# Kernel optimization log

Hardware: AMD Instinct MI355X
Metric: run time of the kernel (lower is better)

Reference implementation:

```python
import jax, jax.numpy as jnp
import numpy as np

B, S, E, H = 16, 512, 4096, 8
HD = E // H  # 512, must equal S for this module's math
LN_EPS = 1e-5
NORM_EPS = 1e-12


def setup_inputs() -> dict:
    key = jax.random.key(0)
    ks = jax.random.split(key, 16)
    s_e = 1.0 / np.sqrt(E)
    s_h = 1.0 / np.sqrt(HD)
    return {
        "x": jax.random.normal(ks[0], (B, S, E), jnp.float32),
        "Wq": jax.random.normal(ks[1], (E, E), jnp.float32) * s_e,
        "bq": jnp.zeros((E,), jnp.float32),
        "Wk": jax.random.normal(ks[2], (E, E), jnp.float32) * s_e,
        "bk": jnp.zeros((E,), jnp.float32),
        "Wv": jax.random.normal(ks[3], (E, E), jnp.float32) * s_e,
        "bv": jnp.zeros((E,), jnp.float32),
        "g_q": jnp.ones((HD,), jnp.float32),
        "b_q": jnp.zeros((HD,), jnp.float32),
        "g_k": jnp.ones((HD,), jnp.float32),
        "b_k": jnp.zeros((HD,), jnp.float32),
        "Wg": jax.random.normal(ks[4], (2 * HD, HD), jnp.float32) * s_h,
        "bg": jnp.zeros((2 * HD,), jnp.float32),
        "Wo": jax.random.normal(ks[5], (E, E), jnp.float32) * s_e,
        "bo": jnp.zeros((E,), jnp.float32),
    }


def _layernorm(t, g, b):
    mu = jnp.mean(t, axis=-1, keepdims=True)
    var = jnp.mean(jnp.square(t - mu), axis=-1, keepdims=True)
    return (t - mu) * jax.lax.rsqrt(var + LN_EPS) * g + b


def reference(x, Wq, bq, Wk, bk, Wv, bv, g_q, b_q, g_k, b_k, Wg, bg, Wo, bo):
    # projections + head split: [B,H,S,HD]
    def proj(W, bias):
        y = jnp.einsum('bse,fe->bsf', x, W) + bias
        return y.reshape(B, S, H, HD).transpose(0, 2, 1, 3)

    q = proj(Wq, bq)
    k = proj(Wk, bk)
    v = proj(Wv, bv)

    # per-head QK LayerNorm over head_dim
    q = _layernorm(q, g_q, b_q)
    k = _layernorm(k, g_k, b_k)

    # scores [B,H,S,S]; note S == HD by construction
    scores = jnp.einsum('bhsd,bhtd->bhst', q, k) / np.sqrt(HD)

    # GeGLU over last dim (linear HD -> 2*HD, chunk, gelu gate)
    h = jnp.einsum('bhst,ft->bhsf', scores, Wg) + bg
    val, gate = h[..., :HD], h[..., HD:]
    w = val * jax.nn.gelu(gate, approximate=False)

    # L2 normalize over last dim (torch F.normalize p=2)
    norm = jnp.sqrt(jnp.sum(jnp.square(w), axis=-1, keepdims=True))
    w = w / jnp.maximum(norm, NORM_EPS)

    # attention-value matmul: [B,H,S,HD] x [B,H,S,HD] with HD==S
    out = jnp.einsum('bhst,bhtd->bhsd', w, v)
    out = out.transpose(0, 2, 1, 3).reshape(B, S, E)
    return jnp.einsum('bse,fe->bsf', out, Wo) + bo
```

## Files before the change

### kernel.cpp

```cpp
#include <hip/hip_runtime.h>
#include <math.h>

typedef __bf16 bf16x8 __attribute__((ext_vector_type(8)));
typedef float f32x4 __attribute__((ext_vector_type(4)));
typedef short short8 __attribute__((ext_vector_type(8)));
typedef unsigned int uint4v __attribute__((ext_vector_type(4)));

__device__ __forceinline__ float bf2f(unsigned short u) {
  union { unsigned int i; float f; } v; v.i = ((unsigned int)u) << 16; return v.f;
}
__device__ __forceinline__ unsigned short f2bf(float f) {
  union { float fl; unsigned int i; } v; v.fl = f;
  unsigned int x = v.i;
  return (unsigned short)((x + 0x7FFFu + ((x >> 16) & 1u)) >> 16);
}
__device__ __forceinline__ unsigned int cvt_pk_bf16(float lo, float hi) {
  unsigned int r;
  asm("v_cvt_pk_bf16_f32 %0, %1, %2" : "=v"(r) : "v"(lo), "v"(hi));
  return r;
}
__device__ __forceinline__ void gl_lds16(const unsigned short* g, void* l) {
  __builtin_amdgcn_global_load_lds(
      (const __attribute__((address_space(1))) unsigned int*)g,
      (__attribute__((address_space(3))) unsigned int*)l, 16, 0, 0);
}

template<int BATCH, int SPLIT3, int CF32, int HAS_BIAS>
__global__ __launch_bounds__(512)
void gemm256(const unsigned short* __restrict__ A,
             const unsigned short* __restrict__ B,
             const float* __restrict__ b0, const float* __restrict__ b1,
             const float* __restrict__ b2,
             void* __restrict__ C0, void* __restrict__ C1, void* __restrict__ C2,
             int K, int lda, int ldb, int ldc, int nbn, float alpha,
             long sAo, long sAi, int nAi,
             long sBo, long sBi, int nBi,
             long sCo, long sCi, int nCi)
{
  __shared__ alignas(16) unsigned char LDS[131072];
  const int NT = K >> 6;

  int tm, tn;
  long offA = 0, offB = 0, offC = 0;
  if (BATCH) {
    const int bx = (int)blockIdx.x;
    tm = (bx / nbn) * 256;
    tn = (bx % nbn) * 256;
    const int z = (int)blockIdx.z;
    offA = (long)(z / nAi) * sAo + (long)(z % nAi) * sAi;
    offB = (long)(z / nBi) * sBo + (long)(z % nBi) * sBi;
    offC = (long)(z / nCi) * sCo + (long)(z % nCi) * sCi;
  } else {
    const int nwg = (int)gridDim.x;
    const int bid = (int)blockIdx.x;
    const int s = (bid & 7) * (nwg >> 3) + (bid >> 3);
    const int sTile = s >> 4, w = s & 15;
    const int snb = nbn >> 2;
    tm = ((sTile / snb) * 4 + (w >> 2)) * 256;
    tn = ((sTile % snb) * 4 + (w & 3)) * 256;
  }

  const int tid = (int)threadIdx.x;
  const int lane = tid & 63;
  const int wv = tid >> 6;
  const int wm = wv >> 2;
  const int wn = wv & 3;
  const int l16 = lane & 15;
  const int kg = lane >> 4;

  const int srow = tid >> 3;
  const int scolb = ((tid & 7) * 16) ^ (((tid >> 3) & 7) << 4);
  const unsigned short* Abase = A + offA + (long)tm * lda + (scolb >> 1);
  const unsigned short* Bbase = B + offB + (long)tn * ldb + (scolb >> 1);
  const int ldsw = wv * 1024;

  const int colswz0 = (kg * 16) ^ ((l16 & 7) << 4);
  const int colswz1 = (64 + kg * 16) ^ ((l16 & 7) << 4);

  f32x4 acc[8][4];
  #pragma unroll
  for (int i = 0; i < 8; ++i)
    #pragma unroll
    for (int j = 0; j < 4; ++j)
      #pragma unroll
      for (int e = 0; e < 4; ++e) acc[i][j][e] = 0.f;

  auto stageA = [&](int t) {
    const int buf = t & 1;
    #pragma unroll
    for (int h = 0; h < 2; ++h)
      #pragma unroll
      for (int i = 0; i < 2; ++i)
        gl_lds16(Abase + (long)(h * 128 + srow + i * 64) * lda + t * 64,
                 &LDS[buf * 32768 + h * 16384 + i * 8192 + ldsw]);
  };
  auto stageBh = [&](int t, int h) {
    const int buf = t & 1;
    #pragma unroll
    for (int i = 0; i < 2; ++i)
      gl_lds16(Bbase + (long)(h * 128 + srow + i * 64) * ldb + t * 64,
               &LDS[65536 + buf * 32768 + h * 16384 + i * 8192 + ldsw]);
  };

  stageA(0); stageBh(0, 0); stageBh(0, 1);
  stageA(1); stageBh(1, 0); stageBh(1, 1);
  asm volatile("s_waitcnt vmcnt(8)" ::: "memory");
  __builtin_amdgcn_s_barrier();

  for (int t = 0; t < NT; ++t) {
    const unsigned char* aB = &LDS[(t & 1) * 32768 + wm * 16384];
    const unsigned char* bB = &LDS[65536 + (t & 1) * 32768 + (wn >> 1) * 16384];
    const int brow = (wn & 1) * 64;
    bf16x8 bfrag[4][2];
    #pragma unroll
    for (int j = 0; j < 4; ++j) {
      bf16x8 a0k0 = *(const bf16x8*)(aB + ((2 * j + 0) * 16 + l16) * 128 + colswz0);
      bf16x8 a0k1 = *(const bf16x8*)(aB + ((2 * j + 0) * 16 + l16) * 128 + colswz1);
      bf16x8 a1k0 = *(const bf16x8*)(aB + ((2 * j + 1) * 16 + l16) * 128 + colswz0);
      bf16x8 a1k1 = *(const bf16x8*)(aB + ((2 * j + 1) * 16 + l16) * 128 + colswz1);
      if (j == 0) {
        #pragma unroll
        for (int ni = 0; ni < 4; ++ni) {
          bfrag[ni][0] = *(const bf16x8*)(bB + (brow + ni * 16 + l16) * 128 + colswz0);
          bfrag[ni][1] = *(const bf16x8*)(bB + (brow + ni * 16 + l16) * 128 + colswz1);
        }
        if (t > 0 && t + 1 < NT) stageA(t + 1);
      } else if (j == 1) {
        if (t + 2 < NT) stageBh(t + 2, 0);
      } else if (j == 2) {
        if (t + 2 < NT) stageBh(t + 2, 1);
      }
      __builtin_amdgcn_s_barrier();
      asm volatile("s_waitcnt lgkmcnt(0)" ::: "memory");
      __builtin_amdgcn_sched_barrier(0);
      __builtin_amdgcn_s_setprio(1);
      #pragma unroll
      for (int ni = 0; ni < 4; ++ni) {
        acc[2 * j + 0][ni] = __builtin_amdgcn_mfma_f32_16x16x32_bf16(a0k0, bfrag[ni][0], acc[2 * j + 0][ni], 0, 0, 0);
        acc[2 * j + 0][ni] = __builtin_amdgcn_mfma_f32_16x16x32_bf16(a0k1, bfrag[ni][1], acc[2 * j + 0][ni], 0, 0, 0);
        acc[2 * j + 1][ni] = __builtin_amdgcn_mfma_f32_16x16x32_bf16(a1k0, bfrag[ni][0], acc[2 * j + 1][ni], 0, 0, 0);
        acc[2 * j + 1][ni] = __builtin_amdgcn_mfma_f32_16x16x32_bf16(a1k1, bfrag[ni][1], acc[2 * j + 1][ni], 0, 0, 0);
      }
      __builtin_amdgcn_s_setprio(0);
      if (j == 3) {
        if (t >= NT - 2) { asm volatile("s_waitcnt vmcnt(0)" ::: "memory"); }
        else             { asm volatile("s_waitcnt vmcnt(4)" ::: "memory"); }
        __builtin_amdgcn_sched_barrier(0);
      }
      __builtin_amdgcn_s_barrier();
    }
  }

  const int which = SPLIT3 ? (tn >> 12) : 0;
  const float* bp = SPLIT3 ? (which == 0 ? b0 : (which == 1 ? b1 : b2)) : b0;
  void* Cp = SPLIT3 ? (which == 0 ? C0 : (which == 1 ? C1 : C2)) : C0;
  const int tnn = SPLIT3 ? (tn & 4095) : tn;
  #pragma unroll
  for (int ni = 0; ni < 4; ++ni) {
    const int col = tnn + wn * 64 + ni * 16 + l16;
    const float bv = HAS_BIAS ? bp[col] : 0.f;
    #pragma unroll
    for (int mi = 0; mi < 8; ++mi) {
      #pragma unroll
      for (int jj = 0; jj < 4; ++jj) {
        const int row = tm + wm * 128 + mi * 16 + kg * 4 + jj;
        const float v = acc[mi][ni][jj] * alpha + bv;
        if (CF32) ((float*)Cp)[offC + (long)row * ldc + col] = v;
        else ((unsigned short*)Cp)[offC + (long)row * ldc + col] = f2bf(v);
      }
    }
  }
}

__global__ __launch_bounds__(256)
void cvt_bf16(const float* __restrict__ in, unsigned short* __restrict__ out, long n8)
{
  long i = (long)blockIdx.x * 256 + threadIdx.x;
  const long stride = (long)gridDim.x * 256;
  for (; i < n8; i += stride) {
    f32x4 v0 = *(const f32x4*)(in + i * 8);
    f32x4 v1 = *(const f32x4*)(in + i * 8 + 4);
    uint4v o;
    o[0] = cvt_pk_bf16(v0[0], v0[1]);
    o[1] = cvt_pk_bf16(v0[2], v0[3]);
    o[2] = cvt_pk_bf16(v1[0], v1[1]);
    o[3] = cvt_pk_bf16(v1[2], v1[3]);
    *(uint4v*)(out + i * 8) = o;
  }
}

__global__ __launch_bounds__(256)
void ln_rows(unsigned short* __restrict__ t, const float* __restrict__ g,
             const float* __restrict__ b)
{
  const int row = blockIdx.x * 4 + ((int)threadIdx.x >> 6);
  const int lane = (int)threadIdx.x & 63;
  unsigned short* p = t + (long)row * 512 + lane * 8;
  short8 rv = *(const short8*)p;
  float x[8];
  #pragma unroll
  for (int j = 0; j < 8; ++j) x[j] = bf2f((unsigned short)rv[j]);
  float s = 0.f;
  #pragma unroll
  for (int j = 0; j < 8; ++j) s += x[j];
  #pragma unroll
  for (int off = 32; off > 0; off >>= 1) s += __shfl_xor(s, off, 64);
  float mu = s * (1.f / 512.f);
  float vs = 0.f;
  #pragma unroll
  for (int j = 0; j < 8; ++j) { float d = x[j] - mu; vs += d * d; }
  #pragma unroll
  for (int off = 32; off > 0; off >>= 1) vs += __shfl_xor(vs, off, 64);
  float rs = rsqrtf(vs * (1.f / 512.f) + 1e-5f);
  f32x4 gv0 = *(const f32x4*)(g + lane * 8);
  f32x4 gv1 = *(const f32x4*)(g + lane * 8 + 4);
  f32x4 bv0 = *(const f32x4*)(b + lane * 8);
  f32x4 bv1 = *(const f32x4*)(b + lane * 8 + 4);
  short8 ov;
  #pragma unroll
  for (int j = 0; j < 4; ++j) ov[j] = (short)f2bf((x[j] - mu) * rs * gv0[j] + bv0[j]);
  #pragma unroll
  for (int j = 0; j < 4; ++j) ov[4 + j] = (short)f2bf((x[4 + j] - mu) * rs * gv1[j] + bv1[j]);
  *(short8*)p = ov;
}

__global__ __launch_bounds__(256)
void gate_norm(const unsigned short* __restrict__ h, unsigned short* __restrict__ w)
{
  const int row = blockIdx.x * 4 + ((int)threadIdx.x >> 6);
  const int lane = (int)threadIdx.x & 63;
  const unsigned short* hp = h + (long)row * 1024 + lane * 8;
  short8 vv = *(const short8*)hp;
  short8 gg = *(const short8*)(hp + 512);
  float wv[8];
  float ssq = 0.f;
  #pragma unroll
  for (int j = 0; j < 8; ++j) {
    float val = bf2f((unsigned short)vv[j]);
    float gt  = bf2f((unsigned short)gg[j]);
    float tt  = val * (0.5f * gt * (1.f + erff(gt * 0.70710678118654752f)));
    wv[j] = tt;
    ssq += tt * tt;
  }
  #pragma unroll
  for (int off = 32; off > 0; off >>= 1) ssq += __shfl_xor(ssq, off, 64);
  float scale = 1.f / fmaxf(sqrtf(ssq), 1e-12f);
  short8 ov;
  #pragma unroll
  for (int j = 0; j < 8; ++j) ov[j] = (short)f2bf(wv[j] * scale);
  *(short8*)(w + (long)row * 512 + lane * 8) = ov;
}

__global__ __launch_bounds__(256)
void transpose_v(const unsigned short* __restrict__ v, unsigned short* __restrict__ vT)
{
  __shared__ alignas(16) unsigned short lt[64][72];
  const int bh = blockIdx.z;
  const int b = bh >> 3, hh = bh & 7;
  const int d0 = blockIdx.x * 64, t0 = blockIdx.y * 64;
  const int tid = (int)threadIdx.x;
  const unsigned short* src = v + (long)b * (512L * 4096L) + hh * 512;
  #pragma unroll
  for (int it = 0; it < 2; ++it) {
    int ci = it * 256 + tid;
    int r = ci >> 3, c8 = (ci & 7) * 8;
    *(short8*)&lt[r][c8] = *(const short8*)(src + (long)(t0 + r) * 4096 + d0 + c8);
  }
  __syncthreads();
  unsigned short* dst = vT + ((long)bh * 512 + d0) * 512 + t0;
  #pragma unroll
  for (int it = 0; it < 2; ++it) {
    int ci = it * 256 + tid;
    int rr = ci >> 3, c8 = (ci & 7) * 8;
    short8 o;
    #pragma unroll
    for (int j = 0; j < 8; ++j) o[j] = (short)lt[c8 + j][rr];
    *(short8*)(dst + (long)rr * 512 + c8) = o;
  }
}

extern "C" void kernel_launch(void* const* d_in, const int* in_sizes, int n_in,
                              void* d_out, int out_size, void* d_ws, size_t ws_size,
                              hipStream_t stream)
{
  (void)in_sizes; (void)n_in; (void)out_size; (void)ws_size;
  const float* x   = (const float*)d_in[0];
  const float* Wq  = (const float*)d_in[1];
  const float* bq  = (const float*)d_in[2];
  const float* Wk  = (const float*)d_in[3];
  const float* bk  = (const float*)d_in[4];
  const float* Wv  = (const float*)d_in[5];
  const float* bv  = (const float*)d_in[6];
  const float* g_q = (const float*)d_in[7];
  const float* b_q = (const float*)d_in[8];
  const float* g_k = (const float*)d_in[9];
  const float* b_k = (const float*)d_in[10];
  const float* Wg  = (const float*)d_in[11];
  const float* bg  = (const float*)d_in[12];
  const float* Wo  = (const float*)d_in[13];
  const float* bo  = (const float*)d_in[14];
  float* out = (float*)d_out;

  const long NE  = 33554432L;
  const long NE2 = NE / 2;
  unsigned short* ws    = (unsigned short*)d_ws;
  unsigned short* xb    = ws;
  unsigned short* Wqkv  = ws + NE;
  unsigned short* qbuf  = ws + NE + 3 * NE2;
  unsigned short* kbuf  = qbuf + NE;
  unsigned short* vbuf  = kbuf + NE;
  unsigned short* Wgb   = Wqkv;
  unsigned short* Wob   = Wqkv + 524288;
  unsigned short* sbuf  = xb;
  unsigned short* vT    = qbuf;
  unsigned short* hbuf  = kbuf;
  unsigned short* wbuf  = xb;
  unsigned short* obuf  = kbuf;

  dim3 blk256(256), blk512(512);
  const float isq = 0.044194173824159216f;

  cvt_bf16<<<16384, blk256, 0, stream>>>(x, xb, NE / 8);
  cvt_bf16<<<8192, blk256, 0, stream>>>(Wq, Wqkv, NE2 / 8);
  cvt_bf16<<<8192, blk256, 0, stream>>>(Wk, Wqkv + NE2, NE2 / 8);
  cvt_bf16<<<8192, blk256, 0, stream>>>(Wv, Wqkv + 2 * NE2, NE2 / 8);

  gemm256<0, 1, 0, 1><<<1536, blk512, 0, stream>>>(
      xb, Wqkv, bq, bk, bv, qbuf, kbuf, vbuf,
      4096, 4096, 4096, 4096, 48, 1.f,
      0L, 0L, 1, 0L, 0L, 1, 0L, 0L, 1);

  cvt_bf16<<<256, blk256, 0, stream>>>(Wg, Wgb, 524288L / 8);
  cvt_bf16<<<8192, blk256, 0, stream>>>(Wo, Wob, NE2 / 8);

  ln_rows<<<16384, blk256, 0, stream>>>(qbuf, g_q, b_q);
  ln_rows<<<16384, blk256, 0, stream>>>(kbuf, g_k, b_k);

  gemm256<1, 0, 0, 0><<<dim3(4, 1, 128), blk512, 0, stream>>>(
      qbuf, kbuf, nullptr, nullptr, nullptr, sbuf, nullptr, nullptr,
      512, 4096, 4096, 512, 2, isq,
      2097152L, 512L, 8,
      2097152L, 512L, 8,
      262144L, 0L, 1);

  transpose_v<<<dim3(8, 8, 128), blk256, 0, stream>>>(vbuf, vT);

  gemm256<1, 0, 0, 1><<<dim3(8, 1, 128), blk512, 0, stream>>>(
      sbuf, Wgb, bg, nullptr, nullptr, hbuf, nullptr, nullptr,
      512, 512, 512, 1024, 4, 1.f,
      262144L, 0L, 1,
      0L, 0L, 1,
      524288L, 0L, 1);

  gate_norm<<<16384, blk256, 0, stream>>>(hbuf, wbuf);

  gemm256<1, 0, 0, 0><<<dim3(4, 1, 128), blk512, 0, stream>>>(
      wbuf, vT, nullptr, nullptr, nullptr, obuf, nullptr, nullptr,
      512, 512, 512, 4096, 2, 1.f,
      262144L, 0L, 1,
      262144L, 0L, 1,
      2097152L, 512L, 8);

  gemm256<0, 0, 1, 1><<<512, blk512, 0, stream>>>(
      obuf, Wob, bo, nullptr, nullptr, out, nullptr, nullptr,
      4096, 4096, 4096, 4096, 16, 1.f,
      0L, 0L, 1, 0L, 0L, 1, 0L, 0L, 1);
}
```

Measured before the change: 1.428 ms.

## Spread A-tile prefetch across k-steps and stage bf16 epilogue through LDS

```diff
diff --git a/kernel.cpp b/kernel.cpp
--- a/kernel.cpp
+++ b/kernel.cpp
@@ -85,14 +85,12 @@
       #pragma unroll
       for (int e = 0; e < 4; ++e) acc[i][j][e] = 0.f;
 
-  auto stageA = [&](int t) {
+  auto stageAh = [&](int t, int h) {
     const int buf = t & 1;
     #pragma unroll
-    for (int h = 0; h < 2; ++h)
-      #pragma unroll
-      for (int i = 0; i < 2; ++i)
-        gl_lds16(Abase + (long)(h * 128 + srow + i * 64) * lda + t * 64,
-                 &LDS[buf * 32768 + h * 16384 + i * 8192 + ldsw]);
+    for (int i = 0; i < 2; ++i)
+      gl_lds16(Abase + (long)(h * 128 + srow + i * 64) * lda + t * 64,
+               &LDS[buf * 32768 + h * 16384 + i * 8192 + ldsw]);
   };
   auto stageBh = [&](int t, int h) {
     const int buf = t & 1;
@@ -102,8 +100,8 @@
                &LDS[65536 + buf * 32768 + h * 16384 + i * 8192 + ldsw]);
   };
 
-  stageA(0); stageBh(0, 0); stageBh(0, 1);
-  stageA(1); stageBh(1, 0); stageBh(1, 1);
+  stageAh(0, 0); stageAh(0, 1); stageBh(0, 0); stageBh(0, 1);
+  stageAh(1, 0); stageAh(1, 1); stageBh(1, 0); stageBh(1, 1);
   asm volatile("s_waitcnt vmcnt(8)" ::: "memory");
   __builtin_amdgcn_s_barrier();
 
@@ -124,10 +122,13 @@
           bfrag[ni][0] = *(const bf16x8*)(bB + (brow + ni * 16 + l16) * 128 + colswz0);
           bfrag[ni][1] = *(const bf16x8*)(bB + (brow + ni * 16 + l16) * 128 + colswz1);
         }
-        if (t > 0 && t + 1 < NT) stageA(t + 1);
+        if (t > 0 && t + 1 < NT) stageAh(t + 1, 0);
+        asm volatile("s_waitcnt lgkmcnt(8)" ::: "memory");
       } else if (j == 1) {
+        if (t > 0 && t + 1 < NT) stageAh(t + 1, 1);
+      } else if (j == 2) {
         if (t + 2 < NT) stageBh(t + 2, 0);
-      } else if (j == 2) {
+      } else {
         if (t + 2 < NT) stageBh(t + 2, 1);
       }
       __builtin_amdgcn_s_barrier();
@@ -155,19 +156,41 @@
   const float* bp = SPLIT3 ? (which == 0 ? b0 : (which == 1 ? b1 : b2)) : b0;
   void* Cp = SPLIT3 ? (which == 0 ? C0 : (which == 1 ? C1 : C2)) : C0;
   const int tnn = SPLIT3 ? (tn & 4095) : tn;
-  #pragma unroll
-  for (int ni = 0; ni < 4; ++ni) {
-    const int col = tnn + wn * 64 + ni * 16 + l16;
-    const float bv = HAS_BIAS ? bp[col] : 0.f;
-    #pragma unroll
-    for (int mi = 0; mi < 8; ++mi) {
+
+  if (CF32) {
+    #pragma unroll
+    for (int ni = 0; ni < 4; ++ni) {
+      const int col = tnn + wn * 64 + ni * 16 + l16;
+      const float bv = HAS_BIAS ? bp[col] : 0.f;
       #pragma unroll
-      for (int jj = 0; jj < 4; ++jj) {
-        const int row = tm + wm * 128 + mi * 16 + kg * 4 + jj;
-        const float v = acc[mi][ni][jj] * alpha + bv;
-        if (CF32) ((float*)Cp)[offC + (long)row * ldc + col] = v;
-        else ((unsigned short*)Cp)[offC + (long)row * ldc + col] = f2bf(v);
-      }
+      for (int mi = 0; mi < 8; ++mi)
+        #pragma unroll
+        for (int jj = 0; jj < 4; ++jj) {
+          const int row = tm + wm * 128 + mi * 16 + kg * 4 + jj;
+          ((float*)Cp)[offC + (long)row * ldc + col] = acc[mi][ni][jj] * alpha + bv;
+        }
+    }
+  } else {
+    unsigned short* lw = (unsigned short*)&LDS[wv * 16384];
+    #pragma unroll
+    for (int ni = 0; ni < 4; ++ni) {
+      const float bv = HAS_BIAS ? bp[tnn + wn * 64 + ni * 16 + l16] : 0.f;
+      #pragma unroll
+      for (int mi = 0; mi < 8; ++mi)
+        #pragma unroll
+        for (int jj = 0; jj < 4; ++jj)
+          lw[(mi * 16 + kg * 4 + jj) * 64 + ni * 16 + l16] =
+              f2bf(acc[mi][ni][jj] * alpha + bv);
+    }
+    asm volatile("s_waitcnt lgkmcnt(0)" ::: "memory");
+    __builtin_amdgcn_sched_barrier(0);
+    unsigned short* Cg = (unsigned short*)Cp + offC +
+                         (long)(tm + wm * 128) * ldc + tnn + wn * 64;
+    const int rr = lane >> 3, cc = (lane & 7) * 8;
+    #pragma unroll
+    for (int i = 0; i < 16; ++i) {
+      short8 val = *(const short8*)&lw[(i * 8 + rr) * 64 + cc];
+      *(short8*)(Cg + (long)(i * 8 + rr) * ldc + cc) = val;
     }
   }
 }
```

Measured after the change: 1.338 ms. 6.3% less time.
